# Kernel optimization log

Hardware: AMD Instinct MI355X
Metric: run time of the kernel (lower is better)

## Reference

```python
import jax, jax.numpy as jnp
import numpy as np

B, N, C = 8, 4096, 256
HEADS, SR = 8, 4
LN_EPS = 1e-5

def setup_inputs() -> dict:
    key = jax.random.key(0)
    ks = jax.random.split(key, 8)
    std = 0.02
    x = jax.random.normal(ks[0], (B, N, C), dtype=jnp.float32)
    q_w = jax.random.normal(ks[1], (C, C), dtype=jnp.float32) * std          # [in,out]
    kv_w = jax.random.normal(ks[2], (C, 2 * C), dtype=jnp.float32) * std     # [in,2*out]
    fan_out = SR * SR * C
    sr_w = jax.random.normal(ks[3], (C, C, SR, SR), dtype=jnp.float32) * np.sqrt(2.0 / fan_out)  # OIHW
    sr_b = jnp.zeros((C,), dtype=jnp.float32)
    ln_w = jnp.ones((C,), dtype=jnp.float32)
    ln_b = jnp.zeros((C,), dtype=jnp.float32)
    proj_w = jax.random.normal(ks[4], (C, C), dtype=jnp.float32) * std
    proj_b = jnp.zeros((C,), dtype=jnp.float32)
    return {"x": x, "H": 64, "W": 64, "q_w": q_w, "kv_w": kv_w, "sr_w": sr_w,
            "sr_b": sr_b, "ln_w": ln_w, "ln_b": ln_b, "proj_w": proj_w, "proj_b": proj_b}


def reference(x, H, W, q_w, kv_w, sr_w, sr_b, ln_w, ln_b, proj_w, proj_b):
    Bb, Nn, Cc = x.shape
    hd = Cc // HEADS
    scale = hd ** -0.5
    # q: [B, heads, N, hd]
    q = (x @ q_w).reshape(Bb, Nn, HEADS, hd).transpose(0, 2, 1, 3)
    # spatial reduction: conv(stride=sr) + LayerNorm
    x_ = x.transpose(0, 2, 1).reshape(Bb, Cc, H, W)
    x_ = jax.lax.conv_general_dilated(
        x_, sr_w, window_strides=(SR, SR), padding="VALID",
        dimension_numbers=("NCHW", "OIHW", "NCHW")) + sr_b[None, :, None, None]
    x_ = x_.reshape(Bb, Cc, -1).transpose(0, 2, 1)  # [B, Nk, C]
    mu = x_.mean(-1, keepdims=True)
    var = x_.var(-1, keepdims=True)
    x_ = (x_ - mu) * jax.lax.rsqrt(var + LN_EPS) * ln_w + ln_b
    # kv: [B, Nk, 2, heads, hd]
    Nk = x_.shape[1]
    kv = (x_ @ kv_w).reshape(Bb, Nk, 2, HEADS, hd)
    k = kv[:, :, 0].transpose(0, 2, 1, 3)  # [B, heads, Nk, hd]
    v = kv[:, :, 1].transpose(0, 2, 1, 3)  # [B, heads, Nk, hd]
    attn = jnp.einsum("bhnd,bhmd->bhnm", q, k) * scale
    attn = jax.nn.softmax(attn, axis=-1)
    out = jnp.einsum("bhnm,bhmd->bhnd", attn, v)  # [B, heads, N, hd]
    out = out.transpose(0, 2, 1, 3).reshape(Bb, Nn, Cc)
    return out @ proj_w + proj_b
```

## Files before the change

kernel.cpp:

```cpp
#include <hip/hip_runtime.h>
#include <hip/hip_bf16.h>
#include <math.h>

#define DI __device__ __forceinline__

static constexpr float SCALE = 0.17677669529663687f;

typedef short bf16x8 __attribute__((ext_vector_type(8)));
typedef float f32x4 __attribute__((ext_vector_type(4)));

__device__ unsigned short g_qwh[256 * 256],  g_qwl[256 * 256];
__device__ unsigned short g_kvwh[512 * 256], g_kvwl[512 * 256];
__device__ unsigned short g_pwh[256 * 256],  g_pwl[256 * 256];
__device__ unsigned short g_wth[(size_t)256 * 4096];
__device__ unsigned short g_wtl[(size_t)256 * 4096];
__device__ unsigned short g_q[(size_t)64 * 4096 * 32];
__device__ unsigned short g_k[(size_t)64 * 256 * 32];
__device__ unsigned short g_vt[(size_t)64 * 32 * 256];
__device__ unsigned short g_convp[(size_t)16 * 2048 * 256];
__device__ unsigned short g_lnh[2048 * 256], g_lnl[2048 * 256];
__device__ unsigned short g_attnb[(size_t)32768 * 256];

DI float bfbits2f(unsigned short b) { return __uint_as_float(((unsigned)b) << 16); }

DI unsigned short f2bf(float f) {
  unsigned u = __float_as_uint(f);
  unsigned r = (u + 0x7fffu + ((u >> 16) & 1u)) >> 16;
  return (unsigned short)r;
}

DI float4 ld_bf4(const unsigned short* p) {
  ushort4 u = *(const ushort4*)p;
  return make_float4(bfbits2f(u.x), bfbits2f(u.y), bfbits2f(u.z), bfbits2f(u.w));
}

DI float ld1(const void* p, size_t i, int f32) {
  return f32 ? ((const float*)p)[i] : bfbits2f(((const unsigned short*)p)[i]);
}

DI float4 ld4(const void* p, size_t i, int f32) {
  if (f32) return *(const float4*)((const float*)p + i);
  return ld_bf4((const unsigned short*)p + i);
}

DI int detect_f32(const void* xp) {
  const unsigned* p = (const unsigned*)xp;
  unsigned m0 = 0, m1 = 0;
#pragma unroll
  for (int i = 0; i < 32; ++i) {
    unsigned w = p[i];
    unsigned lo = w & 0x7fffu, hi = (w >> 16) & 0x7fffu;
    m0 = lo > m0 ? lo : m0;
    m1 = hi > m1 ? hi : m1;
  }
  unsigned mm = m0 > m1 ? m0 : m1;
  return mm >= 0x4680u ? 1 : 0;
}

__global__ void k_prep(const void* __restrict__ qw, const void* __restrict__ kvw,
                       const void* __restrict__ pwp, const void* __restrict__ srw,
                       const void* __restrict__ xp) {
  const int f32 = detect_f32(xp);
  int bid = blockIdx.x;
  if (bid < 1024) {
    int e = bid * 256 + threadIdx.x;
    float v;
    unsigned short *dh, *dl;
    size_t di;
    if (e < 65536) {
      int o = e >> 8, c = e & 255;
      v = ld1(qw, (size_t)c * 256 + o, f32) * SCALE;
      dh = g_qwh; dl = g_qwl; di = e;
    } else if (e < 196608) {
      int e2 = e - 65536;
      int o = e2 >> 8, c = e2 & 255;
      v = ld1(kvw, (size_t)c * 512 + o, f32);
      dh = g_kvwh; dl = g_kvwl; di = e2;
    } else {
      int e2 = e - 196608;
      int o = e2 >> 8, c = e2 & 255;
      v = ld1(pwp, (size_t)c * 256 + o, f32);
      dh = g_pwh; dl = g_pwl; di = e2;
    }
    unsigned short hi = f2bf(v);
    dh[di] = hi;
    dl[di] = f2bf(v - bfbits2f(hi));
  } else {
    int e = (bid - 1024) * 256 + threadIdx.x;
    int o = e >> 12, kk = e & 4095;
    int tap = kk >> 8, ci = kk & 255;
    float v = ld1(srw, (size_t)o * 4096 + ci * 16 + tap, f32);
    unsigned short hi = f2bf(v);
    g_wth[e] = hi;
    g_wtl[e] = f2bf(v - bfbits2f(hi));
  }
}

template <int MODE>
__launch_bounds__(256, 3)
__global__ void k_mgemm(const void* __restrict__ Ax,
                        const void* __restrict__ biasp, void* __restrict__ outp) {
  constexpr bool XIN = (MODE == 0 || MODE == 1);
  constexpr bool AH  = (MODE != 3);
  constexpr int BKROW = (MODE == 1) ? 4096 : 256;

  __shared__ __align__(16) short sa_h[64 * 40];
  __shared__ __align__(16) short sa_l[64 * 40];
  __shared__ __align__(16) short sb_h[256 * 40];
  __shared__ __align__(16) short sb_l[256 * 40];

  int f32 = 0;
  if constexpr (XIN || MODE == 3) f32 = detect_f32(Ax);

  const int tid = threadIdx.x;
  const int m0 = blockIdx.x * 64;
  const int nblk = (MODE == 2) ? blockIdx.y : 0;
  const int kz = (MODE == 1) ? blockIdx.z * 256 : 0;
  const int wave = tid >> 6, lane = tid & 63;
  const int quad = lane >> 4, l15 = lane & 15;

  const unsigned short* Bh = (MODE == 0) ? g_qwh : (MODE == 1) ? g_wth
                           : (MODE == 2) ? g_kvwh : g_pwh;
  const unsigned short* Bl = (MODE == 0) ? g_qwl : (MODE == 1) ? g_wtl
                           : (MODE == 2) ? g_kvwl : g_pwl;

  f32x4 acc[4][4] = {};

  for (int it = 0; it < 8; ++it) {
    const int kb = kz + it * 32;
    {
      int row = tid >> 2, chunk = tid & 3;
      size_t src;
      if constexpr (MODE == 1) {
        int m = m0 + row;
        int bb = m >> 8, sp = m & 255;
        int oh = sp >> 4, ow = sp & 15;
        int tap = kb >> 8, kh = tap >> 2, kw = tap & 3;
        int n = (4 * oh + kh) * 64 + 4 * ow + kw;
        src = (((size_t)(bb * 4096 + n)) << 8) + (kb & 255) + chunk * 8;
      } else {
        src = (((size_t)(m0 + row)) << 8) + kb + chunk * 8;
      }
      if constexpr (XIN) {
        float4 v0 = ld4(Ax, src, f32);
        float4 v1 = ld4(Ax, src + 4, f32);
        ushort4 h0, l0, h1, l1;
        h0.x = f2bf(v0.x); l0.x = f2bf(v0.x - bfbits2f(h0.x));
        h0.y = f2bf(v0.y); l0.y = f2bf(v0.y - bfbits2f(h0.y));
        h0.z = f2bf(v0.z); l0.z = f2bf(v0.z - bfbits2f(h0.z));
        h0.w = f2bf(v0.w); l0.w = f2bf(v0.w - bfbits2f(h0.w));
        h1.x = f2bf(v1.x); l1.x = f2bf(v1.x - bfbits2f(h1.x));
        h1.y = f2bf(v1.y); l1.y = f2bf(v1.y - bfbits2f(h1.y));
        h1.z = f2bf(v1.z); l1.z = f2bf(v1.z - bfbits2f(h1.z));
        h1.w = f2bf(v1.w); l1.w = f2bf(v1.w - bfbits2f(h1.w));
        *(ushort4*)&sa_h[row * 40 + chunk * 8]     = h0;
        *(ushort4*)&sa_h[row * 40 + chunk * 8 + 4] = h1;
        *(ushort4*)&sa_l[row * 40 + chunk * 8]     = l0;
        *(ushort4*)&sa_l[row * 40 + chunk * 8 + 4] = l1;
      } else if constexpr (MODE == 2) {
        *(uint4*)&sa_h[row * 40 + chunk * 8] = *(const uint4*)&g_lnh[src];
        *(uint4*)&sa_l[row * 40 + chunk * 8] = *(const uint4*)&g_lnl[src];
      } else {
        *(uint4*)&sa_h[row * 40 + chunk * 8] = *(const uint4*)&g_attnb[src];
      }
    }
    {
#pragma unroll
      for (int i = 0; i < 4; ++i) {
        int lin = tid + 256 * i;
        int row = lin >> 2, chk = lin & 3;
        size_t src = (size_t)(nblk * 256 + row) * BKROW + kb + chk * 8;
        *(uint4*)&sb_h[row * 40 + chk * 8] = *(const uint4*)&Bh[src];
        *(uint4*)&sb_l[row * 40 + chk * 8] = *(const uint4*)&Bl[src];
      }
    }
    __syncthreads();
#pragma unroll
    for (int mt = 0; mt < 4; ++mt) {
      bf16x8 a_h = *(const bf16x8*)&sa_h[(mt * 16 + l15) * 40 + quad * 8];
      bf16x8 a_l;
      if constexpr (AH) a_l = *(const bf16x8*)&sa_l[(mt * 16 + l15) * 40 + quad * 8];
#pragma unroll
      for (int j = 0; j < 4; ++j) {
        int nr = (4 * wave + j) * 16 + l15;
        bf16x8 b_h = *(const bf16x8*)&sb_h[nr * 40 + quad * 8];
        bf16x8 b_l = *(const bf16x8*)&sb_l[nr * 40 + quad * 8];
        f32x4 c = acc[mt][j];
        c = __builtin_amdgcn_mfma_f32_16x16x32_bf16(a_h, b_h, c, 0, 0, 0);
        if constexpr (AH)
          c = __builtin_amdgcn_mfma_f32_16x16x32_bf16(a_l, b_h, c, 0, 0, 0);
        c = __builtin_amdgcn_mfma_f32_16x16x32_bf16(a_h, b_l, c, 0, 0, 0);
        acc[mt][j] = c;
      }
    }
    __syncthreads();
  }

  const int f32o = f32;
#pragma unroll
  for (int mt = 0; mt < 4; ++mt) {
#pragma unroll
    for (int j = 0; j < 4; ++j) {
#pragma unroll
      for (int r = 0; r < 4; ++r) {
        int m = m0 + mt * 16 + quad * 4 + r;
        int c = nblk * 256 + (4 * wave + j) * 16 + l15;
        float v = acc[mt][j][r];
        if constexpr (MODE == 0) {
          int b = m >> 12, n = m & 4095;
          int h = c >> 5, d = c & 31;
          g_q[(((size_t)(b * 8 + h) * 4096 + n) << 5) + d] = f2bf(v);
        } else if constexpr (MODE == 1) {
          g_convp[((size_t)blockIdx.z * 2048 + m) * 256 + c] = f2bf(v);
        } else if constexpr (MODE == 2) {
          int s = c >> 8, h = (c >> 5) & 7, d = c & 31;
          int bb = m >> 8, nk = m & 255;
          if (s == 0)
            g_k[(((size_t)(bb * 8 + h) * 256 + nk) << 5) + d] = f2bf(v);
          else
            g_vt[(((size_t)(bb * 8 + h) * 32 + d) << 8) + nk] = f2bf(v);
        } else {
          float rr = v + ld1(biasp, c, f32o);
          if (f32o) ((float*)outp)[(size_t)m * 256 + c] = rr;
          else      ((unsigned short*)outp)[(size_t)m * 256 + c] = f2bf(rr);
        }
      }
    }
  }
}

__global__ void k_redln(const void* __restrict__ xp, const void* __restrict__ srb,
                        const void* __restrict__ lw, const void* __restrict__ lb) {
  const int f32 = detect_f32(xp);
  int row = blockIdx.x, t = threadIdx.x;
  size_t idx = (size_t)row * 256 + t;
  float v = 0.f;
#pragma unroll
  for (int z = 0; z < 16; ++z) v += bfbits2f(g_convp[(size_t)z * (2048 * 256) + idx]);
  v += ld1(srb, t, f32);
  float s = v, sq = v * v;
#pragma unroll
  for (int off = 32; off >= 1; off >>= 1) {
    s += __shfl_down(s, off, 64);
    sq += __shfl_down(sq, off, 64);
  }
  __shared__ float rs[4], rq[4];
  int wid = t >> 6;
  if ((t & 63) == 0) { rs[wid] = s; rq[wid] = sq; }
  __syncthreads();
  float st = rs[0] + rs[1] + rs[2] + rs[3];
  float qt = rq[0] + rq[1] + rq[2] + rq[3];
  float mu = st * (1.0f / 256.0f);
  float var = qt * (1.0f / 256.0f) - mu * mu;
  float r = rsqrtf(var + 1e-5f);
  float o = (v - mu) * r * ld1(lw, t, f32) + ld1(lb, t, f32);
  unsigned short hi = f2bf(o);
  g_lnh[idx] = hi;
  g_lnl[idx] = f2bf(o - bfbits2f(hi));
}

__launch_bounds__(256, 4)
__global__ void k_attn() {
  __shared__ short smem[18688];
  short* sk  = smem;
  short* svt = smem + 10240;

  const int tid = threadIdx.x;
  const int bh = blockIdx.y;
  const int b = bh >> 3, h = bh & 7;

  {
    const uint4* gk = (const uint4*)(g_k + (size_t)bh * 8192);
    const uint4* gv = (const uint4*)(g_vt + (size_t)bh * 8192);
    for (int i = tid; i < 1024; i += 256) {
      int key = i >> 2, part = i & 3;
      *(uint4*)&sk[key * 40 + part * 8] = gk[i];
      int d = i >> 5, off = (i & 31) * 8;
      *(uint4*)&svt[d * 264 + off] = gv[i];
    }
  }
  __syncthreads();

  const int wave = tid >> 6, lane = tid & 63;
  const int quad = lane >> 4, l15 = lane & 15;
  const int n0 = blockIdx.x * 64 + wave * 16;

  bf16x8 qv = *(const bf16x8*)(g_q + ((size_t)bh * 4096 + n0 + l15) * 32 + quad * 8);

  f32x4 sacc[16];
#pragma unroll
  for (int t = 0; t < 16; ++t) {
    bf16x8 kf = *(const bf16x8*)&sk[(t * 16 + l15) * 40 + quad * 8];
    f32x4 c = {0.f, 0.f, 0.f, 0.f};
    sacc[t] = __builtin_amdgcn_mfma_f32_16x16x32_bf16(kf, qv, c, 0, 0, 0);
  }

  float m = sacc[0][0];
#pragma unroll
  for (int t = 0; t < 16; ++t) {
#pragma unroll
    for (int r = 0; r < 4; ++r) m = fmaxf(m, sacc[t][r]);
  }
  m = fmaxf(m, __shfl_xor(m, 16, 64));
  m = fmaxf(m, __shfl_xor(m, 32, 64));

  unsigned plo[16], phi[16];
  float ls = 0.f;
#pragma unroll
  for (int t = 0; t < 16; ++t) {
    unsigned short p0 = f2bf(__expf(sacc[t][0] - m));
    unsigned short p1 = f2bf(__expf(sacc[t][1] - m));
    unsigned short p2 = f2bf(__expf(sacc[t][2] - m));
    unsigned short p3 = f2bf(__expf(sacc[t][3] - m));
    ls += bfbits2f(p0) + bfbits2f(p1) + bfbits2f(p2) + bfbits2f(p3);
    plo[t] = (unsigned)p0 | ((unsigned)p1 << 16);
    phi[t] = (unsigned)p2 | ((unsigned)p3 << 16);
  }
  ls += __shfl_xor(ls, 16, 64);
  ls += __shfl_xor(ls, 32, 64);
  float inv = 1.0f / ls;

  f32x4 o0 = {0.f, 0.f, 0.f, 0.f}, o1 = {0.f, 0.f, 0.f, 0.f};
  const int laneA = ((quad & 1) << 5) + l15;
  const int laneB = laneA + 16;
  const bool hiT = quad >= 2;
#pragma unroll
  for (int c = 0; c < 8; ++c) {
    unsigned a0 = __shfl(plo[2 * c], laneA, 64), b0 = __shfl(plo[2 * c + 1], laneA, 64);
    unsigned a1 = __shfl(phi[2 * c], laneA, 64), b1 = __shfl(phi[2 * c + 1], laneA, 64);
    unsigned a2 = __shfl(plo[2 * c], laneB, 64), b2 = __shfl(plo[2 * c + 1], laneB, 64);
    unsigned a3 = __shfl(phi[2 * c], laneB, 64), b3 = __shfl(phi[2 * c + 1], laneB, 64);
    uint4 pk = make_uint4(hiT ? b0 : a0, hiT ? b1 : a1, hiT ? b2 : a2, hiT ? b3 : a3);
    bf16x8 pf = *(bf16x8*)&pk;
    bf16x8 v0 = *(const bf16x8*)&svt[l15 * 264 + c * 32 + quad * 8];
    bf16x8 v1 = *(const bf16x8*)&svt[(16 + l15) * 264 + c * 32 + quad * 8];
    o0 = __builtin_amdgcn_mfma_f32_16x16x32_bf16(v0, pf, o0, 0, 0, 0);
    o1 = __builtin_amdgcn_mfma_f32_16x16x32_bf16(v1, pf, o1, 0, 0, 0);
  }

  size_t base = ((size_t)(b * 4096 + n0 + l15)) * 256 + h * 32 + quad * 4;
  ushort4 u0, u1;
  u0.x = f2bf(o0[0] * inv); u0.y = f2bf(o0[1] * inv);
  u0.z = f2bf(o0[2] * inv); u0.w = f2bf(o0[3] * inv);
  u1.x = f2bf(o1[0] * inv); u1.y = f2bf(o1[1] * inv);
  u1.z = f2bf(o1[2] * inv); u1.w = f2bf(o1[3] * inv);
  *(ushort4*)&g_attnb[base]      = u0;
  *(ushort4*)&g_attnb[base + 16] = u1;
}

extern "C" void kernel_launch(void* const* d_in, const int* in_sizes, int n_in,
                              void* d_out, int out_size, void* d_ws, size_t ws_size,
                              hipStream_t stream) {
  const void* x   = d_in[0];
  const void* qw  = d_in[3];
  const void* kvw = d_in[4];
  const void* srw = d_in[5];
  const void* srb = d_in[6];
  const void* lnw = d_in[7];
  const void* lnb = d_in[8];
  const void* pw  = d_in[9];
  const void* pb  = d_in[10];

  k_prep<<<5120, 256, 0, stream>>>(qw, kvw, pw, srw, x);
  k_mgemm<0><<<dim3(512, 1), 256, 0, stream>>>(x, nullptr, nullptr);
  k_mgemm<1><<<dim3(32, 1, 16), 256, 0, stream>>>(x, nullptr, nullptr);
  k_redln<<<2048, 256, 0, stream>>>(x, srb, lnw, lnb);
  k_mgemm<2><<<dim3(32, 2), 256, 0, stream>>>(nullptr, nullptr, nullptr);
  k_attn<<<dim3(64, 64), 256, 0, stream>>>();
  k_mgemm<3><<<dim3(512, 1), 256, 0, stream>>>(x, pb, d_out);
}
```

Before: 235.6 us.

## Pre-split x into bf16 hi/lo swizzled tiles and load GEMM operands via global_load_lds

The prep kernel now converts x once into an interleaved hi/lo bf16 layout (64-element k-tiles with swizzled slots), and weights and LayerNorm output are stored in the same layout. The GEMM kernels then stream A and B tiles straight into LDS with global_load_lds, dropping the per-block fp32-to-bf16 split of x and the register round-trip for staging. XOR-swizzled LDS offsets are meant to avoid bank conflicts in place of the padded strides. The cost is an extra full pass over x in prep that writes a 32 MB intermediate, and the direct-to-LDS path still has no double buffering.

After: 217.0 us. 1.09x faster.

```diff
diff --git a/kernel.cpp b/kernel.cpp
--- a/kernel.cpp
+++ b/kernel.cpp
@@ -9,16 +9,16 @@
 typedef short bf16x8 __attribute__((ext_vector_type(8)));
 typedef float f32x4 __attribute__((ext_vector_type(4)));
 
-__device__ unsigned short g_qwh[256 * 256],  g_qwl[256 * 256];
-__device__ unsigned short g_kvwh[512 * 256], g_kvwl[512 * 256];
-__device__ unsigned short g_pwh[256 * 256],  g_pwl[256 * 256];
-__device__ unsigned short g_wth[(size_t)256 * 4096];
-__device__ unsigned short g_wtl[(size_t)256 * 4096];
+__device__ unsigned short g_qw2[(size_t)256 * 8 * 64];
+__device__ unsigned short g_kvw2[(size_t)512 * 8 * 64];
+__device__ unsigned short g_pw2[(size_t)256 * 8 * 64];
+__device__ unsigned short g_wt2[(size_t)256 * 128 * 64];
+__device__ unsigned short g_x2[(size_t)32768 * 8 * 64];
+__device__ unsigned short g_ln2[(size_t)2048 * 8 * 64];
 __device__ unsigned short g_q[(size_t)64 * 4096 * 32];
 __device__ unsigned short g_k[(size_t)64 * 256 * 32];
 __device__ unsigned short g_vt[(size_t)64 * 32 * 256];
 __device__ unsigned short g_convp[(size_t)16 * 2048 * 256];
-__device__ unsigned short g_lnh[2048 * 256], g_lnl[2048 * 256];
 __device__ unsigned short g_attnb[(size_t)32768 * 256];
 
 DI float bfbits2f(unsigned short b) { return __uint_as_float(((unsigned)b) << 16); }
@@ -41,6 +41,12 @@
 DI float4 ld4(const void* p, size_t i, int f32) {
   if (f32) return *(const float4*)((const float*)p + i);
   return ld_bf4((const unsigned short*)p + i);
+}
+
+typedef const __attribute__((address_space(1))) void* gas_p;
+typedef __attribute__((address_space(3))) void* las_p;
+DI void gload16(const unsigned short* g, short* l) {
+  __builtin_amdgcn_global_load_lds((gas_p)g, (las_p)l, 16, 0, 0);
 }
 
 DI int detect_f32(const void* xp) {
@@ -61,130 +67,152 @@
                        const void* __restrict__ pwp, const void* __restrict__ srw,
                        const void* __restrict__ xp) {
   const int f32 = detect_f32(xp);
-  int bid = blockIdx.x;
-  if (bid < 1024) {
-    int e = bid * 256 + threadIdx.x;
-    float v;
-    unsigned short *dh, *dl;
-    size_t di;
-    if (e < 65536) {
-      int o = e >> 8, c = e & 255;
-      v = ld1(qw, (size_t)c * 256 + o, f32) * SCALE;
-      dh = g_qwh; dl = g_qwl; di = e;
-    } else if (e < 196608) {
-      int e2 = e - 65536;
-      int o = e2 >> 8, c = e2 & 255;
-      v = ld1(kvw, (size_t)c * 512 + o, f32);
-      dh = g_kvwh; dl = g_kvwl; di = e2;
-    } else {
-      int e2 = e - 196608;
-      int o = e2 >> 8, c = e2 & 255;
-      v = ld1(pwp, (size_t)c * 256 + o, f32);
-      dh = g_pwh; dl = g_pwl; di = e2;
-    }
-    unsigned short hi = f2bf(v);
-    dh[di] = hi;
-    dl[di] = f2bf(v - bfbits2f(hi));
+  int tidg = blockIdx.x * 256 + threadIdx.x;
+  float v[8];
+  unsigned short* dst;
+  if (tidg < 8192) {
+    int o = tidg >> 5, w = tidg & 31, k = w * 8;
+#pragma unroll
+    for (int j = 0; j < 8; ++j) v[j] = ld1(qw, (size_t)(k + j) * 256 + o, f32) * SCALE;
+    dst = g_qw2 + ((size_t)o * 8 + (w >> 2)) * 64 + (w & 3) * 8;
+  } else if (tidg < 24576) {
+    int t = tidg - 8192;
+    int o = t >> 5, w = t & 31, k = w * 8;
+#pragma unroll
+    for (int j = 0; j < 8; ++j) v[j] = ld1(kvw, (size_t)(k + j) * 512 + o, f32);
+    dst = g_kvw2 + ((size_t)o * 8 + (w >> 2)) * 64 + (w & 3) * 8;
+  } else if (tidg < 32768) {
+    int t = tidg - 24576;
+    int o = t >> 5, w = t & 31, k = w * 8;
+#pragma unroll
+    for (int j = 0; j < 8; ++j) v[j] = ld1(pwp, (size_t)(k + j) * 256 + o, f32);
+    dst = g_pw2 + ((size_t)o * 8 + (w >> 2)) * 64 + (w & 3) * 8;
+  } else if (tidg < 163840) {
+    int t = tidg - 32768;
+    int o = t >> 9, w = t & 511, k = w * 8;
+#pragma unroll
+    for (int j = 0; j < 8; ++j) {
+      int kk = k + j, tap = kk >> 8, ci = kk & 255;
+      v[j] = ld1(srw, (size_t)o * 4096 + (size_t)ci * 16 + tap, f32);
+    }
+    dst = g_wt2 + ((size_t)o * 128 + (w >> 2)) * 64 + (w & 3) * 8;
   } else {
-    int e = (bid - 1024) * 256 + threadIdx.x;
-    int o = e >> 12, kk = e & 4095;
-    int tap = kk >> 8, ci = kk & 255;
-    float v = ld1(srw, (size_t)o * 4096 + ci * 16 + tap, f32);
-    unsigned short hi = f2bf(v);
-    g_wth[e] = hi;
-    g_wtl[e] = f2bf(v - bfbits2f(hi));
-  }
+    int t = tidg - 163840;
+    int m = t >> 5, w = t & 31, k = w * 8;
+    size_t base = (size_t)m * 256 + k;
+    float4 a = ld4(xp, base, f32);
+    float4 b = ld4(xp, base + 4, f32);
+    v[0] = a.x; v[1] = a.y; v[2] = a.z; v[3] = a.w;
+    v[4] = b.x; v[5] = b.y; v[6] = b.z; v[7] = b.w;
+    dst = g_x2 + ((size_t)m * 8 + (w >> 2)) * 64 + (w & 3) * 8;
+  }
+  ushort4 h0, h1, l0, l1;
+  h0.x = f2bf(v[0]); l0.x = f2bf(v[0] - bfbits2f(h0.x));
+  h0.y = f2bf(v[1]); l0.y = f2bf(v[1] - bfbits2f(h0.y));
+  h0.z = f2bf(v[2]); l0.z = f2bf(v[2] - bfbits2f(h0.z));
+  h0.w = f2bf(v[3]); l0.w = f2bf(v[3] - bfbits2f(h0.w));
+  h1.x = f2bf(v[4]); l1.x = f2bf(v[4] - bfbits2f(h1.x));
+  h1.y = f2bf(v[5]); l1.y = f2bf(v[5] - bfbits2f(h1.y));
+  h1.z = f2bf(v[6]); l1.z = f2bf(v[6] - bfbits2f(h1.z));
+  h1.w = f2bf(v[7]); l1.w = f2bf(v[7] - bfbits2f(h1.w));
+  *(ushort4*)dst        = h0;
+  *(ushort4*)(dst + 4)  = h1;
+  *(ushort4*)(dst + 32) = l0;
+  *(ushort4*)(dst + 36) = l1;
 }
 
 template <int MODE>
 __launch_bounds__(256, 3)
 __global__ void k_mgemm(const void* __restrict__ Ax,
                         const void* __restrict__ biasp, void* __restrict__ outp) {
-  constexpr bool XIN = (MODE == 0 || MODE == 1);
-  constexpr bool AH  = (MODE != 3);
-  constexpr int BKROW = (MODE == 1) ? 4096 : 256;
-
-  __shared__ __align__(16) short sa_h[64 * 40];
-  __shared__ __align__(16) short sa_l[64 * 40];
-  __shared__ __align__(16) short sb_h[256 * 40];
-  __shared__ __align__(16) short sb_l[256 * 40];
+  constexpr bool AH = (MODE != 3);
+  constexpr int ASZ = AH ? 4096 : 2048;
+  __shared__ __align__(16) short smem[ASZ + 16384];
+  short* sa = smem;
+  short* sb = smem + ASZ;
 
   int f32 = 0;
-  if constexpr (XIN || MODE == 3) f32 = detect_f32(Ax);
+  if constexpr (MODE == 3) f32 = detect_f32(Ax);
 
   const int tid = threadIdx.x;
   const int m0 = blockIdx.x * 64;
   const int nblk = (MODE == 2) ? blockIdx.y : 0;
-  const int kz = (MODE == 1) ? blockIdx.z * 256 : 0;
+  const int z = (MODE == 1) ? blockIdx.z : 0;
   const int wave = tid >> 6, lane = tid & 63;
   const int quad = lane >> 4, l15 = lane & 15;
 
-  const unsigned short* Bh = (MODE == 0) ? g_qwh : (MODE == 1) ? g_wth
-                           : (MODE == 2) ? g_kvwh : g_pwh;
-  const unsigned short* Bl = (MODE == 0) ? g_qwl : (MODE == 1) ? g_wtl
-                           : (MODE == 2) ? g_kvwl : g_pwl;
+  const int srow = tid >> 3;
+  const int slot = (tid & 7) ^ (srow & 7);
+
+  size_t abase0 = 0, abase1 = 0;
+  if constexpr (MODE == 0 || MODE == 2) {
+    abase0 = ((size_t)(m0 + srow) * 8) * 64 + slot * 8;
+    abase1 = ((size_t)(m0 + 32 + srow) * 8) * 64 + slot * 8;
+  } else if constexpr (MODE == 1) {
+    const int kh = z >> 2, kw = z & 3;
+#pragma unroll
+    for (int r = 0; r < 2; ++r) {
+      int m = m0 + r * 32 + srow;
+      int bb = m >> 8, sp = m & 255;
+      int oh = sp >> 4, ow = sp & 15;
+      int n = (4 * oh + kh) * 64 + 4 * ow + kw;
+      size_t ab = ((size_t)(bb * 4096 + n) * 8) * 64 + slot * 8;
+      if (r == 0) abase0 = ab; else abase1 = ab;
+    }
+  } else {
+    int ar = tid >> 2;
+    int s3 = (tid & 3) ^ (ar & 3);
+    abase0 = (size_t)(m0 + ar) * 256 + s3 * 8;
+  }
+
+  const unsigned short* Asrc =
+      (MODE == 0 || MODE == 1) ? g_x2 : (MODE == 2) ? g_ln2 : g_attnb;
+  const unsigned short* Bsrc = (MODE == 0) ? g_qw2 : (MODE == 1) ? g_wt2
+                             : (MODE == 2) ? g_kvw2 : g_pw2;
+  constexpr int NKT = (MODE == 1) ? 128 : 8;
+  const size_t bbase =
+      ((size_t)(nblk * 256 + srow) * NKT + (MODE == 1 ? z * 8 : 0)) * 64 + slot * 8;
+
+  short* adst0 = sa + wave * 512 + lane * 8;
+  short* adst1 = sa + 2048 + wave * 512 + lane * 8;
+  short* bdst  = sb + wave * 512 + lane * 8;
+
+  int aoff[4], boff[4];
+#pragma unroll
+  for (int mt = 0; mt < 4; ++mt) {
+    int ar = mt * 16 + l15;
+    if constexpr (AH) aoff[mt] = ar * 64 + ((quad ^ (ar & 7)) << 3);
+    else              aoff[mt] = ar * 32 + ((quad ^ (ar & 3)) << 3);
+  }
+#pragma unroll
+  for (int j = 0; j < 4; ++j) {
+    int br = (4 * wave + j) * 16 + l15;
+    boff[j] = br * 64 + ((quad ^ (br & 7)) << 3);
+  }
 
   f32x4 acc[4][4] = {};
 
   for (int it = 0; it < 8; ++it) {
-    const int kb = kz + it * 32;
-    {
-      int row = tid >> 2, chunk = tid & 3;
-      size_t src;
-      if constexpr (MODE == 1) {
-        int m = m0 + row;
-        int bb = m >> 8, sp = m & 255;
-        int oh = sp >> 4, ow = sp & 15;
-        int tap = kb >> 8, kh = tap >> 2, kw = tap & 3;
-        int n = (4 * oh + kh) * 64 + 4 * ow + kw;
-        src = (((size_t)(bb * 4096 + n)) << 8) + (kb & 255) + chunk * 8;
-      } else {
-        src = (((size_t)(m0 + row)) << 8) + kb + chunk * 8;
-      }
-      if constexpr (XIN) {
-        float4 v0 = ld4(Ax, src, f32);
-        float4 v1 = ld4(Ax, src + 4, f32);
-        ushort4 h0, l0, h1, l1;
-        h0.x = f2bf(v0.x); l0.x = f2bf(v0.x - bfbits2f(h0.x));
-        h0.y = f2bf(v0.y); l0.y = f2bf(v0.y - bfbits2f(h0.y));
-        h0.z = f2bf(v0.z); l0.z = f2bf(v0.z - bfbits2f(h0.z));
-        h0.w = f2bf(v0.w); l0.w = f2bf(v0.w - bfbits2f(h0.w));
-        h1.x = f2bf(v1.x); l1.x = f2bf(v1.x - bfbits2f(h1.x));
-        h1.y = f2bf(v1.y); l1.y = f2bf(v1.y - bfbits2f(h1.y));
-        h1.z = f2bf(v1.z); l1.z = f2bf(v1.z - bfbits2f(h1.z));
-        h1.w = f2bf(v1.w); l1.w = f2bf(v1.w - bfbits2f(h1.w));
-        *(ushort4*)&sa_h[row * 40 + chunk * 8]     = h0;
-        *(ushort4*)&sa_h[row * 40 + chunk * 8 + 4] = h1;
-        *(ushort4*)&sa_l[row * 40 + chunk * 8]     = l0;
-        *(ushort4*)&sa_l[row * 40 + chunk * 8 + 4] = l1;
-      } else if constexpr (MODE == 2) {
-        *(uint4*)&sa_h[row * 40 + chunk * 8] = *(const uint4*)&g_lnh[src];
-        *(uint4*)&sa_l[row * 40 + chunk * 8] = *(const uint4*)&g_lnl[src];
-      } else {
-        *(uint4*)&sa_h[row * 40 + chunk * 8] = *(const uint4*)&g_attnb[src];
-      }
-    }
-    {
-#pragma unroll
-      for (int i = 0; i < 4; ++i) {
-        int lin = tid + 256 * i;
-        int row = lin >> 2, chk = lin & 3;
-        size_t src = (size_t)(nblk * 256 + row) * BKROW + kb + chk * 8;
-        *(uint4*)&sb_h[row * 40 + chk * 8] = *(const uint4*)&Bh[src];
-        *(uint4*)&sb_l[row * 40 + chk * 8] = *(const uint4*)&Bl[src];
-      }
+    if constexpr (AH) {
+      gload16(Asrc + abase0 + it * 64, adst0);
+      gload16(Asrc + abase1 + it * 64, adst1);
+    } else {
+      gload16(Asrc + abase0 + it * 32, adst0);
+    }
+#pragma unroll
+    for (int r = 0; r < 8; ++r) {
+      gload16(Bsrc + bbase + (size_t)r * (32 * NKT * 64) + it * 64, bdst + r * 2048);
     }
     __syncthreads();
 #pragma unroll
     for (int mt = 0; mt < 4; ++mt) {
-      bf16x8 a_h = *(const bf16x8*)&sa_h[(mt * 16 + l15) * 40 + quad * 8];
+      bf16x8 a_h = *(const bf16x8*)&sa[aoff[mt]];
       bf16x8 a_l;
-      if constexpr (AH) a_l = *(const bf16x8*)&sa_l[(mt * 16 + l15) * 40 + quad * 8];
+      if constexpr (AH) a_l = *(const bf16x8*)&sa[aoff[mt] ^ 32];
 #pragma unroll
       for (int j = 0; j < 4; ++j) {
-        int nr = (4 * wave + j) * 16 + l15;
-        bf16x8 b_h = *(const bf16x8*)&sb_h[nr * 40 + quad * 8];
-        bf16x8 b_l = *(const bf16x8*)&sb_l[nr * 40 + quad * 8];
+        bf16x8 b_h = *(const bf16x8*)&sb[boff[j]];
+        bf16x8 b_l = *(const bf16x8*)&sb[boff[j] ^ 32];
         f32x4 c = acc[mt][j];
         c = __builtin_amdgcn_mfma_f32_16x16x32_bf16(a_h, b_h, c, 0, 0, 0);
         if constexpr (AH)
@@ -255,8 +283,9 @@
   float r = rsqrtf(var + 1e-5f);
   float o = (v - mu) * r * ld1(lw, t, f32) + ld1(lb, t, f32);
   unsigned short hi = f2bf(o);
-  g_lnh[idx] = hi;
-  g_lnl[idx] = f2bf(o - bfbits2f(hi));
+  size_t dbase = ((size_t)row * 8 + (t >> 5)) * 64 + (t & 31);
+  g_ln2[dbase]      = hi;
+  g_ln2[dbase + 32] = f2bf(o - bfbits2f(hi));
 }
 
 __launch_bounds__(256, 4)
@@ -361,9 +390,9 @@
   const void* pw  = d_in[9];
   const void* pb  = d_in[10];
 
-  k_prep<<<5120, 256, 0, stream>>>(qw, kvw, pw, srw, x);
-  k_mgemm<0><<<dim3(512, 1), 256, 0, stream>>>(x, nullptr, nullptr);
-  k_mgemm<1><<<dim3(32, 1, 16), 256, 0, stream>>>(x, nullptr, nullptr);
+  k_prep<<<4736, 256, 0, stream>>>(qw, kvw, pw, srw, x);
+  k_mgemm<0><<<dim3(512, 1), 256, 0, stream>>>(nullptr, nullptr, nullptr);
+  k_mgemm<1><<<dim3(32, 1, 16), 256, 0, stream>>>(nullptr, nullptr, nullptr);
   k_redln<<<2048, 256, 0, stream>>>(x, srb, lnw, lnb);
   k_mgemm<2><<<dim3(32, 2), 256, 0, stream>>>(nullptr, nullptr, nullptr);
   k_attn<<<dim3(64, 64), 256, 0, stream>>>();
```
